# Kernel tuning notes

Measured on AMD Instinct MI355X. Metric: run time of the kernel, lower is better.

## Reference

```python
import jax, jax.numpy as jnp
import numpy as np

N_NODES = 50000
VOCAB = 2048
HID = 256
N_EDGES = 1600000


def setup_inputs() -> dict:
    key = jax.random.key(0)
    ks = jax.random.split(key, 7)
    context = jax.random.normal(ks[0], (N_NODES, VOCAB), dtype=jnp.float32)
    adj_row = jax.random.randint(ks[1], (N_EDGES,), 0, N_NODES, dtype=jnp.int64)
    adj_col = jax.random.randint(ks[2], (N_EDGES,), 0, N_NODES, dtype=jnp.int64)
    adj_val = jax.random.uniform(ks[3], (N_EDGES,), dtype=jnp.float32)
    # learned params
    context_weight = jax.random.normal(ks[4], (HID, VOCAB), dtype=jnp.float32) * 0.02
    out_w = jax.random.normal(ks[5], (VOCAB, HID), dtype=jnp.float32) * 0.02
    out_b = jnp.zeros((VOCAB,), dtype=jnp.float32)
    return {
        "context": context,
        "adj_row": adj_row,
        "adj_col": adj_col,
        "adj_val": adj_val,
        "context_weight": context_weight,
        "out_w": out_w,
        "out_b": out_b,
    }


def reference(context, adj_row, adj_col, adj_val, context_weight, out_w, out_b):
    # support = context @ context_weight.T : [N, hid]
    support = jnp.einsum('nv,hv->nh', context, context_weight)
    # spmm: out[r] += val * support[c]  (COO sparse-dense matmul)
    gathered = support[adj_col] * adj_val[:, None]          # [E, hid]
    agg = jax.ops.segment_sum(gathered, adj_row, num_segments=N_NODES)  # [N, hid]
    score = jax.nn.relu(agg)
    # out linear: hid -> vocab
    output = jnp.einsum('nh,vh->nv', score, out_w) + out_b  # [N, vocab]
    return output
```

## Files before the change

### kernel.cpp

```cpp
#include <hip/hip_runtime.h>
#include <hip/hip_bf16.h>

#define N_NODES 50000
#define VOCAB   2048
#define HID     256
#define N_EDGES 1600000

typedef __attribute__((ext_vector_type(8))) __bf16 bf16x8;
typedef __attribute__((ext_vector_type(4))) __bf16 bf16x4;
typedef __attribute__((ext_vector_type(4))) float  f32x4;

__device__ __forceinline__ void gl_lds16(const void* g, void* l) {
    __builtin_amdgcn_global_load_lds(
        (const __attribute__((address_space(1))) void*)g,
        (__attribute__((address_space(3))) void*)l, 16, 0, 0);
}

#define HIST_NB 256
#define CVT_NB  512
__global__ __launch_bounds__(256) void phase1(
    const int*   __restrict__ arow, int* __restrict__ cnt, int E,
    const float* __restrict__ w1, __bf16* __restrict__ w1b,
    const float* __restrict__ w2, __bf16* __restrict__ w2b)
{
    const int tid = threadIdx.x;
    int bid = blockIdx.x;
    if (bid < HIST_NB) {
        const int stride = HIST_NB * 256;
        for (int e4 = bid * 256 + tid; e4 < E / 4; e4 += stride) {
            const int4 r = ((const int4*)arow)[e4];
            atomicAdd(&cnt[r.x], 1); atomicAdd(&cnt[r.y], 1);
            atomicAdd(&cnt[r.z], 1); atomicAdd(&cnt[r.w], 1);
        }
        return;
    }
    bid -= HIST_NB;
    const float* w  = (bid < CVT_NB) ? w1 : w2;
    __bf16*      wb = (bid < CVT_NB) ? w1b : w2b;
    if (bid >= CVT_NB) bid -= CVT_NB;
    const int t = bid * 256 + tid;
    const float4 v = ((const float4*)w)[t];
    bf16x4 p = { (__bf16)v.x, (__bf16)v.y, (__bf16)v.z, (__bf16)v.w };
    ((bf16x4*)wb)[t] = p;
}

#define SCAN_NB 49

__global__ __launch_bounds__(256) void scan1(
    const int* __restrict__ cnt, int* __restrict__ bsum, int n)
{
    __shared__ int red[256];
    const int base = blockIdx.x * 1024 + threadIdx.x * 4;
    int s = 0;
    #pragma unroll
    for (int i = 0; i < 4; ++i) { const int idx = base + i; if (idx < n) s += cnt[idx]; }
    red[threadIdx.x] = s;
    __syncthreads();
    for (int off = 128; off > 0; off >>= 1) {
        if (threadIdx.x < off) red[threadIdx.x] += red[threadIdx.x + off];
        __syncthreads();
    }
    if (threadIdx.x == 0) bsum[blockIdx.x] = red[0];
}

__global__ __launch_bounds__(64) void scan2(int* __restrict__ bsum, int nb)
{
    if (threadIdx.x == 0) {
        int run = 0;
        for (int b = 0; b < nb; ++b) { const int v = bsum[b]; bsum[b] = run; run += v; }
        bsum[nb] = run;
    }
}

__global__ __launch_bounds__(256) void scan3(
    const int* __restrict__ cnt, const int* __restrict__ bsum,
    int* __restrict__ ptr, int* __restrict__ cursor, int n)
{
    __shared__ int hs[256];
    const int base = blockIdx.x * 1024 + threadIdx.x * 4;
    int loc[4]; int s = 0;
    #pragma unroll
    for (int i = 0; i < 4; ++i) {
        const int idx = base + i;
        loc[i] = (idx < n) ? cnt[idx] : 0;
        s += loc[i];
    }
    hs[threadIdx.x] = s;
    __syncthreads();
    for (int off = 1; off < 256; off <<= 1) {
        int v = (threadIdx.x >= off) ? hs[threadIdx.x - off] : 0;
        __syncthreads();
        hs[threadIdx.x] += v;
        __syncthreads();
    }
    int run = bsum[blockIdx.x] + ((threadIdx.x == 0) ? 0 : hs[threadIdx.x - 1]);
    #pragma unroll
    for (int i = 0; i < 4; ++i) {
        const int idx = base + i;
        if (idx < n) { ptr[idx] = run; cursor[idx] = run; }
        run += loc[i];
    }
    if (blockIdx.x == SCAN_NB - 1 && threadIdx.x == 255) ptr[n] = run;
}

#define FILL_NB 256
__global__ __launch_bounds__(256) void fill_gemm1(
    const int*    __restrict__ arow,
    const int*    __restrict__ acol,
    const float*  __restrict__ aval,
    int*          __restrict__ cursor,
    int2*         __restrict__ cpair,
    int E,
    const float*  __restrict__ Af,
    const __bf16* __restrict__ Bb,
    __bf16*       __restrict__ Cb,
    int M)
{
    const int tid = threadIdx.x;
    int bid = blockIdx.x;

    if (bid < FILL_NB) {
        const int stride = FILL_NB * 256;
        for (int e4 = bid * 256 + tid; e4 < E / 4; e4 += stride) {
            const int4   r = ((const int4*)arow)[e4];
            const int4   c = ((const int4*)acol)[e4];
            const float4 v = ((const float4*)aval)[e4];
            int p;
            p = atomicAdd(&cursor[r.x], 1); cpair[p] = make_int2(c.x, __float_as_int(v.x));
            p = atomicAdd(&cursor[r.y], 1); cpair[p] = make_int2(c.y, __float_as_int(v.y));
            p = atomicAdd(&cursor[r.z], 1); cpair[p] = make_int2(c.z, __float_as_int(v.z));
            p = atomicAdd(&cursor[r.w], 1); cpair[p] = make_int2(c.w, __float_as_int(v.w));
        }
        return;
    }
    bid -= FILL_NB;

    constexpr int K = 2048, N = 256, BM = 64, BK = 32, nkt = K / BK;
    __shared__ float sAf[2][BM * BK];

    const int lane = tid & 63;
    const int wn   = tid >> 6;
    const int half = lane >> 4;
    const int r16  = lane & 15;
    const int m0   = bid * BM;

    f32x4 acc[4][4] = {};

    auto stageA = [&](int kt, int b) {
        const int k0 = kt * BK;
        #pragma unroll
        for (int i = 0; i < 2; ++i) {
            const int s   = i * 256 + tid;
            const int row = s >> 3, c = s & 7;
            const int csw = c ^ (row & 7);
            int gr = m0 + row; if (gr >= M) gr = M - 1;
            gl_lds16(&Af[(size_t)gr * K + k0 + csw * 4], &sAf[b][s * 4]);
        }
    };

    stageA(0, 0);
    __syncthreads();
    for (int t = 0; t < nkt; ++t) {
        uint4 bq[4];
        #pragma unroll
        for (int n = 0; n < 4; ++n) {
            const int brow = wn * 64 + n * 16 + r16;
            bq[n] = *(const uint4*)&Bb[(size_t)brow * K + t * BK + half * 8];
        }
        if (t + 1 < nkt) stageA(t + 1, (t + 1) & 1);
        const int b = t & 1;
        #pragma unroll
        for (int m = 0; m < 4; ++m) {
            const int arw = m * 16 + r16;
            const int rx  = arw & 7;
            const f32x4 lo = *(const f32x4*)&sAf[b][arw * 32 + ((2 * half)     ^ rx) * 4];
            const f32x4 hi = *(const f32x4*)&sAf[b][arw * 32 + ((2 * half + 1) ^ rx) * 4];
            const bf16x8 af = { (__bf16)lo.x, (__bf16)lo.y, (__bf16)lo.z, (__bf16)lo.w,
                                (__bf16)hi.x, (__bf16)hi.y, (__bf16)hi.z, (__bf16)hi.w };
            #pragma unroll
            for (int n = 0; n < 4; ++n)
                acc[m][n] = __builtin_amdgcn_mfma_f32_16x16x32_bf16(
                                af, *(const bf16x8*)&bq[n], acc[m][n], 0, 0, 0);
        }
        __syncthreads();
    }

    #pragma unroll
    for (int m = 0; m < 4; ++m) {
        #pragma unroll
        for (int j = 0; j < 4; ++j) {
            const int gr = m0 + m * 16 + half * 4 + j;
            if (gr >= M) continue;
            #pragma unroll
            for (int n = 0; n < 4; ++n) {
                const int gc = wn * 64 + n * 16 + r16;
                Cb[(size_t)gr * N + gc] = (__bf16)acc[m][n][j];
            }
        }
    }
}

__global__ __launch_bounds__(256) void spmm_gather(
    const int*    __restrict__ ptr,
    const int2*   __restrict__ cpair,
    const __bf16* __restrict__ support,
    __bf16*       __restrict__ agg,
    int n)
{
    const int tid  = threadIdx.x;
    const int lane = tid & 63;
    const int row  = blockIdx.x * 4 + (tid >> 6);
    if (row >= n) return;
    const int l32 = lane & 31, ep = lane >> 5;
    const int beg = ptr[row], end = ptr[row + 1];

    float a[8] = {0.f, 0.f, 0.f, 0.f, 0.f, 0.f, 0.f, 0.f};

    auto fma8 = [&](float v, const uint4& s) {
        a[0] += v * __uint_as_float(s.x << 16);
        a[1] += v * __uint_as_float(s.x & 0xFFFF0000u);
        a[2] += v * __uint_as_float(s.y << 16);
        a[3] += v * __uint_as_float(s.y & 0xFFFF0000u);
        a[4] += v * __uint_as_float(s.z << 16);
        a[5] += v * __uint_as_float(s.z & 0xFFFF0000u);
        a[6] += v * __uint_as_float(s.w << 16);
        a[7] += v * __uint_as_float(s.w & 0xFFFF0000u);
    };

    int i = beg;
    for (; i + 8 <= end; i += 8) {
        const int2 p0 = cpair[i + ep];
        const int2 p1 = cpair[i + 2 + ep];
        const int2 p2 = cpair[i + 4 + ep];
        const int2 p3 = cpair[i + 6 + ep];
        const uint4 s0 = *(const uint4*)&support[(size_t)p0.x * HID + l32 * 8];
        const uint4 s1 = *(const uint4*)&support[(size_t)p1.x * HID + l32 * 8];
        const uint4 s2 = *(const uint4*)&support[(size_t)p2.x * HID + l32 * 8];
        const uint4 s3 = *(const uint4*)&support[(size_t)p3.x * HID + l32 * 8];
        fma8(__int_as_float(p0.y), s0);
        fma8(__int_as_float(p1.y), s1);
        fma8(__int_as_float(p2.y), s2);
        fma8(__int_as_float(p3.y), s3);
    }
    for (; i + 2 <= end; i += 2) {
        const int2 p = cpair[i + ep];
        const uint4 s = *(const uint4*)&support[(size_t)p.x * HID + l32 * 8];
        fma8(__int_as_float(p.y), s);
    }
    if (i < end && ep == 0) {
        const int2 p = cpair[i];
        const uint4 s = *(const uint4*)&support[(size_t)p.x * HID + l32 * 8];
        fma8(__int_as_float(p.y), s);
    }

    #pragma unroll
    for (int k = 0; k < 8; ++k) a[k] += __shfl_xor(a[k], 32);

    if (ep == 0) {
        bf16x8 o = { (__bf16)fmaxf(a[0], 0.f), (__bf16)fmaxf(a[1], 0.f),
                     (__bf16)fmaxf(a[2], 0.f), (__bf16)fmaxf(a[3], 0.f),
                     (__bf16)fmaxf(a[4], 0.f), (__bf16)fmaxf(a[5], 0.f),
                     (__bf16)fmaxf(a[6], 0.f), (__bf16)fmaxf(a[7], 0.f) };
        *(bf16x8*)&agg[(size_t)row * HID + l32 * 8] = o;
    }
}

__global__ __launch_bounds__(256) void gemm2(
    const __bf16* __restrict__ Ab,
    const __bf16* __restrict__ Bb,
    const float*  __restrict__ bias,
    float*        __restrict__ C,
    int M)
{
    constexpr int K = 256, N = 2048, BM = 128, BN = 128, BK = 32;
    constexpr int NBY = N / BN, nkt = K / BK;
    __shared__ __bf16 sA[2][BM * BK];

    const int tid  = threadIdx.x;
    const int lane = tid & 63;
    const int wid  = tid >> 6;
    const int wm   = wid >> 1;
    const int wn   = wid & 1;
    const int half = lane >> 4;
    const int r16  = lane & 15;

    const int nwg = gridDim.x, cpx = nwg >> 3;
    const int wg  = (blockIdx.x & 7) * cpx + (blockIdx.x >> 3);
    const int m0  = (wg / NBY) * BM;
    const int n0  = (wg % NBY) * BN;

    f32x4 acc[4][4] = {};

    auto stageA = [&](int kt, int b) {
        const int k0 = kt * BK;
        #pragma unroll
        for (int i = 0; i < 2; ++i) {
            const int s   = i * 256 + tid;
            const int row = s >> 2, c = s & 3;
            const int csw = c ^ (row & 3);
            int gr = m0 + row; if (gr >= M) gr = M - 1;
            gl_lds16(&Ab[(size_t)gr * K + k0 + csw * 8], &sA[b][s * 8]);
        }
    };

    stageA(0, 0);
    __syncthreads();
    for (int t = 0; t < nkt; ++t) {
        uint4 bq[4];
        #pragma unroll
        for (int n = 0; n < 4; ++n) {
            const int brow = n0 + wn * 64 + n * 16 + r16;
            bq[n] = *(const uint4*)&Bb[(size_t)brow * K + t * BK + half * 8];
        }
        if (t + 1 < nkt) stageA(t + 1, (t + 1) & 1);
        const int b = t & 1;
        #pragma unroll
        for (int m = 0; m < 4; ++m) {
            const int arw = wm * 64 + m * 16 + r16;
            const bf16x8 af = *(const bf16x8*)&sA[b][arw * 32 + (half ^ (arw & 3)) * 8];
            #pragma unroll
            for (int n = 0; n < 4; ++n)
                acc[m][n] = __builtin_amdgcn_mfma_f32_16x16x32_bf16(
                                af, *(const bf16x8*)&bq[n], acc[m][n], 0, 0, 0);
        }
        __syncthreads();
    }

    #pragma unroll
    for (int m = 0; m < 4; ++m) {
        #pragma unroll
        for (int j = 0; j < 4; ++j) {
            const int gr = m0 + wm * 64 + m * 16 + half * 4 + j;
            if (gr >= M) continue;
            #pragma unroll
            for (int n = 0; n < 4; ++n) {
                const int gc = n0 + wn * 64 + n * 16 + r16;
                __builtin_nontemporal_store(acc[m][n][j] + bias[gc],
                                            &C[(size_t)gr * N + gc]);
            }
        }
    }
}

extern "C" void kernel_launch(void* const* d_in, const int* in_sizes, int n_in,
                              void* d_out, int out_size, void* d_ws, size_t ws_size,
                              hipStream_t stream) {
    const float* context  = (const float*)d_in[0];
    const int*   adj_row  = (const int*)  d_in[1];
    const int*   adj_col  = (const int*)  d_in[2];
    const float* adj_val  = (const float*)d_in[3];
    const float* ctx_w    = (const float*)d_in[4];
    const float* out_w    = (const float*)d_in[5];
    const float* out_b    = (const float*)d_in[6];
    float*       out      = (float*)d_out;

    char* ws = (char*)d_ws;
    __bf16* support_b = (__bf16*)ws;  ws += (size_t)N_NODES * HID * 2;
    __bf16* agg_b     = (__bf16*)ws;  ws += (size_t)N_NODES * HID * 2;
    __bf16* ctxw_b    = (__bf16*)ws;  ws += (size_t)HID * VOCAB * 2;
    __bf16* outw_b    = (__bf16*)ws;  ws += (size_t)VOCAB * HID * 2;
    int*    csr_ptr   = (int*)ws;     ws += ((size_t)N_NODES + 16) * 4;
    int*    cnt       = (int*)ws;     ws += (size_t)N_NODES * 4;
    int*    cursor    = (int*)ws;     ws += (size_t)N_NODES * 4;
    int*    bsum      = (int*)ws;     ws += ((size_t)SCAN_NB + 16) * 4;
    int2*   cpair     = (int2*)ws;    ws += (size_t)N_EDGES * 8;

    hipMemsetAsync(cnt, 0, (size_t)N_NODES * 4, stream);

    phase1<<<dim3(HIST_NB + 2 * CVT_NB), 256, 0, stream>>>(
        adj_row, cnt, N_EDGES, ctx_w, ctxw_b, out_w, outw_b);

    scan1<<<SCAN_NB, 256, 0, stream>>>(cnt, bsum, N_NODES);
    scan2<<<1, 64, 0, stream>>>(bsum, SCAN_NB);
    scan3<<<SCAN_NB, 256, 0, stream>>>(cnt, bsum, csr_ptr, cursor, N_NODES);

    fill_gemm1<<<dim3(FILL_NB + (N_NODES + 63) / 64), 256, 0, stream>>>(
        adj_row, adj_col, adj_val, cursor, cpair, N_EDGES,
        context, ctxw_b, support_b, N_NODES);

    spmm_gather<<<(N_NODES + 3) / 4, 256, 0, stream>>>(
        csr_ptr, cpair, support_b, agg_b, N_NODES);

    gemm2<<<dim3(((N_NODES + 127) / 128) * (VOCAB / 128)), 256, 0, stream>>>(
        agg_b, outw_b, out_b, out, N_NODES);
}
```

Baseline: 581.9 us.

## Stage B operands through LDS and triple-buffer gemm2 with vmcnt waits

```diff
diff --git a/kernel.cpp b/kernel.cpp
--- a/kernel.cpp
+++ b/kernel.cpp
@@ -116,6 +116,10 @@
     __bf16*       __restrict__ Cb,
     int M)
 {
+    constexpr int K = 2048, N = 256, BM = 64, BK = 32, nkt = K / BK;
+    __shared__ float  sAf[2][BM * BK];
+    __shared__ __bf16 sB [2][N  * BK];
+
     const int tid = threadIdx.x;
     int bid = blockIdx.x;
 
@@ -135,9 +139,6 @@
     }
     bid -= FILL_NB;
 
-    constexpr int K = 2048, N = 256, BM = 64, BK = 32, nkt = K / BK;
-    __shared__ float sAf[2][BM * BK];
-
     const int lane = tid & 63;
     const int wn   = tid >> 6;
     const int half = lane >> 4;
@@ -146,7 +147,7 @@
 
     f32x4 acc[4][4] = {};
 
-    auto stageA = [&](int kt, int b) {
+    auto stage = [&](int kt, int b) {
         const int k0 = kt * BK;
         #pragma unroll
         for (int i = 0; i < 2; ++i) {
@@ -156,19 +157,21 @@
             int gr = m0 + row; if (gr >= M) gr = M - 1;
             gl_lds16(&Af[(size_t)gr * K + k0 + csw * 4], &sAf[b][s * 4]);
         }
+        #pragma unroll
+        for (int i = 0; i < 4; ++i) {
+            const int s   = i * 256 + tid;
+            const int row = s >> 2, c = s & 3;
+            const int csw = c ^ (row & 3);
+            gl_lds16(&Bb[(size_t)row * K + k0 + csw * 8], &sB[b][s * 8]);
+        }
     };
-
-    stageA(0, 0);
-    __syncthreads();
-    for (int t = 0; t < nkt; ++t) {
-        uint4 bq[4];
+    auto step = [&](int b) {
+        bf16x8 bfr[4];
         #pragma unroll
         for (int n = 0; n < 4; ++n) {
             const int brow = wn * 64 + n * 16 + r16;
-            bq[n] = *(const uint4*)&Bb[(size_t)brow * K + t * BK + half * 8];
-        }
-        if (t + 1 < nkt) stageA(t + 1, (t + 1) & 1);
-        const int b = t & 1;
+            bfr[n] = *(const bf16x8*)&sB[b][brow * 32 + (half ^ (brow & 3)) * 8];
+        }
         #pragma unroll
         for (int m = 0; m < 4; ++m) {
             const int arw = m * 16 + r16;
@@ -180,8 +183,16 @@
             #pragma unroll
             for (int n = 0; n < 4; ++n)
                 acc[m][n] = __builtin_amdgcn_mfma_f32_16x16x32_bf16(
-                                af, *(const bf16x8*)&bq[n], acc[m][n], 0, 0, 0);
-        }
+                                af, bfr[n], acc[m][n], 0, 0, 0);
+        }
+    };
+
+    stage(0, 0);
+    __syncthreads();
+    for (int kt = 0; kt < nkt; ++kt) {
+        const int cur = kt & 1;
+        if (kt + 1 < nkt) stage(kt + 1, cur ^ 1);
+        step(cur);
         __syncthreads();
     }
 
@@ -274,7 +285,8 @@
 {
     constexpr int K = 256, N = 2048, BM = 128, BN = 128, BK = 32;
     constexpr int NBY = N / BN, nkt = K / BK;
-    __shared__ __bf16 sA[2][BM * BK];
+    __shared__ __bf16 sA[3][BM * BK];
+    __shared__ __bf16 sB[3][BN * BK];
 
     const int tid  = threadIdx.x;
     const int lane = tid & 63;
@@ -291,7 +303,7 @@
 
     f32x4 acc[4][4] = {};
 
-    auto stageA = [&](int kt, int b) {
+    auto stage = [&](int kt, int b) {
         const int k0 = kt * BK;
         #pragma unroll
         for (int i = 0; i < 2; ++i) {
@@ -301,19 +313,21 @@
             int gr = m0 + row; if (gr >= M) gr = M - 1;
             gl_lds16(&Ab[(size_t)gr * K + k0 + csw * 8], &sA[b][s * 8]);
         }
+        #pragma unroll
+        for (int i = 0; i < 2; ++i) {
+            const int s   = i * 256 + tid;
+            const int row = s >> 2, c = s & 3;
+            const int csw = c ^ (row & 3);
+            gl_lds16(&Bb[(size_t)(n0 + row) * K + k0 + csw * 8], &sB[b][s * 8]);
+        }
     };
-
-    stageA(0, 0);
-    __syncthreads();
-    for (int t = 0; t < nkt; ++t) {
-        uint4 bq[4];
+    auto step = [&](int b) {
+        bf16x8 bfr[4];
         #pragma unroll
         for (int n = 0; n < 4; ++n) {
-            const int brow = n0 + wn * 64 + n * 16 + r16;
-            bq[n] = *(const uint4*)&Bb[(size_t)brow * K + t * BK + half * 8];
-        }
-        if (t + 1 < nkt) stageA(t + 1, (t + 1) & 1);
-        const int b = t & 1;
+            const int brow = wn * 64 + n * 16 + r16;
+            bfr[n] = *(const bf16x8*)&sB[b][brow * 32 + (half ^ (brow & 3)) * 8];
+        }
         #pragma unroll
         for (int m = 0; m < 4; ++m) {
             const int arw = wm * 64 + m * 16 + r16;
@@ -321,9 +335,19 @@
             #pragma unroll
             for (int n = 0; n < 4; ++n)
                 acc[m][n] = __builtin_amdgcn_mfma_f32_16x16x32_bf16(
-                                af, *(const bf16x8*)&bq[n], acc[m][n], 0, 0, 0);
-        }
-        __syncthreads();
+                                af, bfr[n], acc[m][n], 0, 0, 0);
+        }
+    };
+
+    stage(0, 0);
+    stage(1, 1);
+    for (int t = 0; t < nkt; ++t) {
+        if (t + 1 < nkt) asm volatile("s_waitcnt vmcnt(4)" ::: "memory");
+        else             asm volatile("s_waitcnt vmcnt(0)" ::: "memory");
+        __builtin_amdgcn_s_barrier();
+        __builtin_amdgcn_sched_barrier(0);
+        step(t % 3);
+        if (t + 2 < nkt) stage(t + 2, (t + 2) % 3);
     }
 
     #pragma unroll
```

New measurement: 541.7 us. -6.9%, faster.
